# Kernel tuning notes

Hardware: AMD Instinct MI355X
Metric: run time of the kernel (lower is better)

The kernel has to match this reference:

```python
import jax, jax.numpy as jnp
import numpy as np

KSIZE = 3
STRIDE = 1
PADDING = 1
DILATION = 1
C_IN = 16
C_OUT = 16


def setup_inputs() -> dict:
    key = jax.random.key(0)
    k1, k2, k3 = jax.random.split(key, 3)
    inputs = jax.random.normal(k1, (2, C_IN, 24, 24, 24, 24), dtype=jnp.float32)
    weight = jax.random.normal(k2, (C_OUT, C_IN * KSIZE ** 4), dtype=jnp.float32)
    bias = jax.random.normal(k3, (1, C_OUT, 1, 1, 1, 1), dtype=jnp.float32)
    return {"inputs": inputs, "weight": weight, "bias": bias}


def reference(inputs, weight, bias):
    # weight stored flattened: [C_out, C_in * k^4] -> [C_out, C_in, k, k, k, k]
    w = weight.reshape(C_OUT, C_IN, KSIZE, KSIZE, KSIZE, KSIZE)
    # General 4-spatial-dim convolution via XLA's ND conv.
    dn = jax.lax.ConvDimensionNumbers(
        lhs_spec=(0, 1, 2, 3, 4, 5),   # N, C, U, V, H, W
        rhs_spec=(0, 1, 2, 3, 4, 5),   # O, I, kU, kV, kH, kW
        out_spec=(0, 1, 2, 3, 4, 5),
    )
    out = jax.lax.conv_general_dilated(
        inputs, w,
        window_strides=(STRIDE,) * 4,
        padding=((PADDING, PADDING),) * 4,
        rhs_dilation=(DILATION,) * 4,
        dimension_numbers=dn,
    )
    return out + bias
```

## Files before the change

kernel.cpp:

```cpp
#include <hip/hip_runtime.h>

#define S 24
#define PLANE 576
#define CISTRIDE 331776
#define SLAB_B 21632
#define HSLAB_B 11648
#define HOFF 9984
#define A_BYTES 46080
#define WS_SLABS A_BYTES

typedef __attribute__((ext_vector_type(8))) short bf16x8;
typedef __attribute__((ext_vector_type(4))) float f32x4;

__device__ __forceinline__ ushort f2bf(float f) {
    unsigned int u = __builtin_bit_cast(unsigned int, f);
    unsigned int r = u + 0x7fffu + ((u >> 16) & 1u);
    return (ushort)(r >> 16);
}

__device__ __forceinline__ int swz(int row, int col, int half) {
    return (((row * 26 + col) * 32) + half * 16) ^ ((row & 3) << 4);
}

__global__ void __launch_bounds__(256)
pack_in(const float* __restrict__ in, const float* __restrict__ wgt, char* __restrict__ ws) {
    __shared__ unsigned lds_t[16][288];

    const int b = blockIdx.x;
    const int nb = b / PLANE, uv = b % PLANE;
    const float* src = in + (size_t)nb * 16 * CISTRIDE + (size_t)uv * PLANE;
    char* dst = ws + WS_SLABS + (size_t)b * SLAB_B;
    const int t = threadIdx.x;

    #pragma unroll
    for (int i = 0; i < 9; ++i) {
        int flat = i * 256 + t;
        int ci = flat / 144, q4 = flat % 144;
        float4 f = *(const float4*)(src + (size_t)ci * CISTRIDE + 4 * q4);
        uint2 pk;
        pk.x = (unsigned)f2bf(f.x) | ((unsigned)f2bf(f.y) << 16);
        pk.y = (unsigned)f2bf(f.z) | ((unsigned)f2bf(f.w) << 16);
        *(uint2*)&lds_t[ci][2 * q4] = pk;
    }
    __syncthreads();

    #pragma unroll
    for (int i = 0; i < 6; ++i) {
        int c = i * 256 + t;
        if (c < 1352) {
            int k = c >> 2;
            int row = k / 13;
            int pos2 = c ^ (row & 3);
            int pos = pos2 >> 1, h = pos2 & 1;
            int col = pos - row * 26;
            uint4 o = make_uint4(0, 0, 0, 0);
            if (row >= 1 && row <= 24 && col >= 1 && col <= 24) {
                int q = (row - 1) * 24 + (col - 1);
                int q2 = q >> 1, odd = q & 1;
                #pragma unroll
                for (int kk = 0; kk < 4; ++kk) {
                    unsigned a = lds_t[8 * h + 2 * kk][q2];
                    unsigned bb = lds_t[8 * h + 2 * kk + 1][q2];
                    unsigned val = odd ? ((a >> 16) | (bb & 0xffff0000u))
                                       : ((a & 0xffffu) | (bb << 16));
                    ((unsigned*)&o)[kk] = val;
                }
            }
            *(uint4*)(dst + (size_t)c * 16) = o;
        }
    }

    if (b == 0) {
        for (int i = t; i < 2880; i += 256) {
            int step = i >> 6;
            int tap = step / 5, s = step % 5;
            int lane = i & 63;
            int co = lane & 15, gA = lane >> 4;
            int o = 2 * s + (gA >> 1);
            int cib = (gA & 1) * 8;
            ushort vals[8];
            #pragma unroll
            for (int j = 0; j < 8; ++j)
                vals[j] = (o <= 8) ? f2bf(wgt[co * 1296 + (cib + j) * 81 + tap * 9 + o]) : (ushort)0;
            uint4 pk;
            pk.x = vals[0] | ((unsigned)vals[1] << 16);
            pk.y = vals[2] | ((unsigned)vals[3] << 16);
            pk.z = vals[4] | ((unsigned)vals[5] << 16);
            pk.w = vals[6] | ((unsigned)vals[7] << 16);
            *(uint4*)(ws + (size_t)i * 16) = pk;
        }
    }
}

__global__ void __launch_bounds__(192, 4)
conv4d_main(const char* __restrict__ ws, const float* __restrict__ bias,
            float* __restrict__ out) {
    __shared__ __align__(16) char lds[2 * HSLAB_B];

    const int t = threadIdx.x, lane = t & 63, wvid = t >> 6;
    const int braw = blockIdx.x;
    const int b = (braw & 7) * 144 + (braw >> 3);
    const int nb = b / 576, rem = b % 576;
    const int u = rem / 24, rem2 = rem % 24;
    const int v0 = (rem2 >> 1) * 2, hh = rem2 & 1;

    const int n16 = lane & 15, g = lane >> 4;
    const int dh = n16 >> 3, dw = n16 & 7;
    const int half = g & 1, osel = g >> 1;

    int laneoff[2][5];
    #pragma unroll
    for (int trp = 0; trp < 2; ++trp)
        #pragma unroll
        for (int s = 0; s < 5; ++s) {
            int o = 2 * s + osel; if (o > 8) o = 8;
            int kh = o / 3, kw = o % 3;
            int r_off = dh + kh, c_off = dw + kw;
            int lin = (r_off * 26 + c_off) * 32 + half * 16;
            laneoff[trp][s] = lin ^ ((((trp << 1) + r_off) & 3) << 4);
        }

    f32x4 acc0[6], acc1[6];
    #pragma unroll
    for (int i = 0; i < 6; ++i) { acc0[i] = (f32x4){0,0,0,0}; acc1[i] = (f32x4){0,0,0,0}; }

    unsigned mask = 0;
    #pragma unroll
    for (int i = 0; i < 12; ++i) {
        int uu = u + (i >> 2) - 1, vv = v0 + (i & 3) - 1;
        if (uu >= 0 && uu < S && vv >= 0 && vv < S) mask |= 1u << i;
    }

    const char* slabs = ws + WS_SLABS;
    const int srcoff = hh * HOFF;
    #define SLAB_PTR(i_) (slabs + ((size_t)nb * PLANE + (u + ((i_) >> 2) - 1) * S + (v0 + ((i_) & 3) - 1)) * SLAB_B + srcoff)

    #define STAGE(bufsel_, src_) do {                                              \
        const char* _s = (src_);                                                   \
        _Pragma("unroll")                                                          \
        for (int r2 = 0; r2 < 4; ++r2) {                                           \
            int chunk = r2 * 192 + t;                                              \
            if (r2 < 3 || t < 152)                                                 \
                __builtin_amdgcn_global_load_lds(                                  \
                    (const __attribute__((address_space(1))) unsigned int*)(_s + (size_t)chunk * 16), \
                    (__attribute__((address_space(3))) unsigned int*)(lds + (bufsel_) * HSLAB_B + chunk * 16), \
                    16, 0, 0);                                                     \
        }                                                                          \
    } while (0)

    const bf16x8 zfr = {0,0,0,0,0,0,0,0};

    int cur = __ffs(mask) - 1;
    int bufsel = 0;
    STAGE(0, SLAB_PTR(cur));
    __syncthreads();

    while (1) {
        unsigned remm = mask >> (cur + 1);
        int nxt = remm ? (cur + 1 + __ffs(remm) - 1) : -1;
        if (nxt >= 0) STAGE(bufsel ^ 1, SLAB_PTR(nxt));

        const int ku = cur >> 2, dv = (cur & 3) - 1;
        const bool v0ok = dv <= 1, v1ok = dv >= 0;
        const char* ap0 = ws + (size_t)(ku * 3 + dv + 1) * 5120 + (size_t)lane * 16;
        const char* ap1 = ws + (size_t)(ku * 3 + dv) * 5120 + (size_t)lane * 16;
        bf16x8 afr0[5], afr1[5];
        #pragma unroll
        for (int s = 0; s < 5; ++s) {
            afr0[s] = v0ok ? *(const bf16x8*)(ap0 + s * 1024) : zfr;
            afr1[s] = v1ok ? *(const bf16x8*)(ap1 + s * 1024) : zfr;
        }

        const char* bp = lds + bufsel * HSLAB_B + wvid * 3328;
        #pragma unroll
        for (int tr = 0; tr < 2; ++tr) {
            #pragma unroll
            for (int tc = 0; tc < 3; ++tc) {
                const int ti = tr * 3 + tc;
                const char* bpt = bp + tr * 1664 + tc * 256;
                #pragma unroll
                for (int s = 0; s < 5; ++s) {
                    bf16x8 bfr = *(const bf16x8*)(bpt + laneoff[tr][s]);
                    acc0[ti] = __builtin_amdgcn_mfma_f32_16x16x32_bf16(afr0[s], bfr, acc0[ti], 0, 0, 0);
                    acc1[ti] = __builtin_amdgcn_mfma_f32_16x16x32_bf16(afr1[s], bfr, acc1[ti], 0, 0, 0);
                }
            }
        }
        __syncthreads();
        if (nxt < 0) break;
        cur = nxt; bufsel ^= 1;
    }

    float bv[4];
    #pragma unroll
    for (int r = 0; r < 4; ++r) bv[r] = bias[g * 4 + r];
    float* outp0 = out + (size_t)nb * 16 * CISTRIDE + (size_t)(u * S + v0) * PLANE;
    float* outp1 = outp0 + PLANE;
    #pragma unroll
    for (int tr = 0; tr < 2; ++tr) {
        #pragma unroll
        for (int tc = 0; tc < 3; ++tc) {
            const int ti = tr * 3 + tc;
            int row = hh * 12 + wvid * 4 + tr * 2 + dh;
            int col = tc * 8 + dw;
            int pos = row * S + col;
            #pragma unroll
            for (int r = 0; r < 4; ++r) {
                outp0[(size_t)(g * 4 + r) * CISTRIDE + pos] = acc0[ti][r] + bv[r];
                outp1[(size_t)(g * 4 + r) * CISTRIDE + pos] = acc1[ti][r] + bv[r];
            }
        }
    }
}

extern "C" void kernel_launch(void* const* d_in, const int* in_sizes, int n_in,
                              void* d_out, int out_size, void* d_ws, size_t ws_size,
                              hipStream_t stream) {
    const float* in   = (const float*)d_in[0];
    const float* wgt  = (const float*)d_in[1];
    const float* bias = (const float*)d_in[2];
    float* out        = (float*)d_out;
    char* ws          = (char*)d_ws;

    pack_in<<<dim3(2 * PLANE), dim3(256), 0, stream>>>(in, wgt, ws);
    conv4d_main<<<dim3(1152), dim3(192), 0, stream>>>(ws, bias, out);
}
```

Measured before the change: 77.43 us.

## Split conv work into quarter-slab tiles and half-plane pack blocks for more blocks

The main conv kernel now gives each block a quarter of the HW plane (6 output rows) instead of a half, doubling the grid to 2304 blocks and halving the per-block LDS slab and accumulator count. Each wave covers one 8-column strip across 3 row pairs instead of 2 rows by 3 column tiles. The pack kernel is likewise split so each block handles half a plane, doubling its grid and halving its LDS. This aims for better occupancy and load balance across CUs, at the cost of more redundant halo loading (quarter slabs overlap by halo rows) and more weight-fragment reloads per output.

Measured after the change: 79.18 us. 1.02x slower.

```diff
diff --git a/kernel.cpp b/kernel.cpp
--- a/kernel.cpp
+++ b/kernel.cpp
@@ -4,8 +4,8 @@
 #define PLANE 576
 #define CISTRIDE 331776
 #define SLAB_B 21632
-#define HSLAB_B 11648
-#define HOFF 9984
+#define QSLAB_B 6656
+#define QOFF 4992
 #define A_BYTES 46080
 #define WS_SLABS A_BYTES
 
@@ -18,45 +18,45 @@
     return (ushort)(r >> 16);
 }
 
-__device__ __forceinline__ int swz(int row, int col, int half) {
-    return (((row * 26 + col) * 32) + half * 16) ^ ((row & 3) << 4);
-}
-
 __global__ void __launch_bounds__(256)
 pack_in(const float* __restrict__ in, const float* __restrict__ wgt, char* __restrict__ ws) {
-    __shared__ unsigned lds_t[16][288];
+    __shared__ unsigned lds_t[16][144];
 
     const int b = blockIdx.x;
-    const int nb = b / PLANE, uv = b % PLANE;
-    const float* src = in + (size_t)nb * 16 * CISTRIDE + (size_t)uv * PLANE;
-    char* dst = ws + WS_SLABS + (size_t)b * SLAB_B;
+    const int slab = b >> 1, hhp = b & 1;
+    const int nb = slab / PLANE, uv = slab % PLANE;
+    const float* src = in + (size_t)nb * 16 * CISTRIDE + (size_t)uv * PLANE + hhp * 288;
+    char* dst = ws + WS_SLABS + (size_t)slab * SLAB_B;
     const int t = threadIdx.x;
 
     #pragma unroll
-    for (int i = 0; i < 9; ++i) {
+    for (int i = 0; i < 5; ++i) {
         int flat = i * 256 + t;
-        int ci = flat / 144, q4 = flat % 144;
-        float4 f = *(const float4*)(src + (size_t)ci * CISTRIDE + 4 * q4);
-        uint2 pk;
-        pk.x = (unsigned)f2bf(f.x) | ((unsigned)f2bf(f.y) << 16);
-        pk.y = (unsigned)f2bf(f.z) | ((unsigned)f2bf(f.w) << 16);
-        *(uint2*)&lds_t[ci][2 * q4] = pk;
+        if (flat < 1152) {
+            int ci = flat / 72, q4 = flat % 72;
+            float4 f = *(const float4*)(src + (size_t)ci * CISTRIDE + 4 * q4);
+            uint2 pk;
+            pk.x = (unsigned)f2bf(f.x) | ((unsigned)f2bf(f.y) << 16);
+            pk.y = (unsigned)f2bf(f.z) | ((unsigned)f2bf(f.w) << 16);
+            *(uint2*)&lds_t[ci][2 * q4] = pk;
+        }
     }
     __syncthreads();
 
     #pragma unroll
-    for (int i = 0; i < 6; ++i) {
+    for (int i = 0; i < 3; ++i) {
         int c = i * 256 + t;
-        if (c < 1352) {
-            int k = c >> 2;
-            int row = k / 13;
-            int pos2 = c ^ (row & 3);
+        if (c < 676) {
+            int row_local = c / 52;
+            int row = 13 * hhp + row_local;
+            int cg = 676 * hhp + c;
+            int pos2 = cg ^ (row & 3);
             int pos = pos2 >> 1, h = pos2 & 1;
             int col = pos - row * 26;
             uint4 o = make_uint4(0, 0, 0, 0);
             if (row >= 1 && row <= 24 && col >= 1 && col <= 24) {
-                int q = (row - 1) * 24 + (col - 1);
-                int q2 = q >> 1, odd = q & 1;
+                int ql = (row - 1) * 24 + (col - 1) - hhp * 288;
+                int q2 = ql >> 1, odd = ql & 1;
                 #pragma unroll
                 for (int kk = 0; kk < 4; ++kk) {
                     unsigned a = lds_t[8 * h + 2 * kk][q2];
@@ -66,7 +66,7 @@
                     ((unsigned*)&o)[kk] = val;
                 }
             }
-            *(uint4*)(dst + (size_t)c * 16) = o;
+            *(uint4*)(dst + (size_t)cg * 16) = o;
         }
     }
 
@@ -95,14 +95,14 @@
 __global__ void __launch_bounds__(192, 4)
 conv4d_main(const char* __restrict__ ws, const float* __restrict__ bias,
             float* __restrict__ out) {
-    __shared__ __align__(16) char lds[2 * HSLAB_B];
+    __shared__ __align__(16) char lds[2 * QSLAB_B];
 
     const int t = threadIdx.x, lane = t & 63, wvid = t >> 6;
     const int braw = blockIdx.x;
-    const int b = (braw & 7) * 144 + (braw >> 3);
-    const int nb = b / 576, rem = b % 576;
-    const int u = rem / 24, rem2 = rem % 24;
-    const int v0 = (rem2 >> 1) * 2, hh = rem2 & 1;
+    const int b = (braw & 7) * 288 + (braw >> 3);
+    const int nb = b / 1152, rem = b % 1152;
+    const int u = rem / 48, rem2 = rem % 48;
+    const int v0 = (rem2 >> 2) * 2, qq = rem2 & 3;
 
     const int n16 = lane & 15, g = lane >> 4;
     const int dh = n16 >> 3, dw = n16 & 7;
@@ -120,9 +120,9 @@
             laneoff[trp][s] = lin ^ ((((trp << 1) + r_off) & 3) << 4);
         }
 
-    f32x4 acc0[6], acc1[6];
-    #pragma unroll
-    for (int i = 0; i < 6; ++i) { acc0[i] = (f32x4){0,0,0,0}; acc1[i] = (f32x4){0,0,0,0}; }
+    f32x4 acc0[3], acc1[3];
+    #pragma unroll
+    for (int i = 0; i < 3; ++i) { acc0[i] = (f32x4){0,0,0,0}; acc1[i] = (f32x4){0,0,0,0}; }
 
     unsigned mask = 0;
     #pragma unroll
@@ -132,18 +132,18 @@
     }
 
     const char* slabs = ws + WS_SLABS;
-    const int srcoff = hh * HOFF;
+    const int srcoff = qq * QOFF;
     #define SLAB_PTR(i_) (slabs + ((size_t)nb * PLANE + (u + ((i_) >> 2) - 1) * S + (v0 + ((i_) & 3) - 1)) * SLAB_B + srcoff)
 
     #define STAGE(bufsel_, src_) do {                                              \
         const char* _s = (src_);                                                   \
         _Pragma("unroll")                                                          \
-        for (int r2 = 0; r2 < 4; ++r2) {                                           \
+        for (int r2 = 0; r2 < 3; ++r2) {                                           \
             int chunk = r2 * 192 + t;                                              \
-            if (r2 < 3 || t < 152)                                                 \
+            if (r2 < 2 || t < 32)                                                  \
                 __builtin_amdgcn_global_load_lds(                                  \
                     (const __attribute__((address_space(1))) unsigned int*)(_s + (size_t)chunk * 16), \
-                    (__attribute__((address_space(3))) unsigned int*)(lds + (bufsel_) * HSLAB_B + chunk * 16), \
+                    (__attribute__((address_space(3))) unsigned int*)(lds + (bufsel_) * QSLAB_B + chunk * 16), \
                     16, 0, 0);                                                     \
         }                                                                          \
     } while (0)
@@ -171,19 +171,16 @@
             afr1[s] = v1ok ? *(const bf16x8*)(ap1 + s * 1024) : zfr;
         }
 
-        const char* bp = lds + bufsel * HSLAB_B + wvid * 3328;
-        #pragma unroll
-        for (int tr = 0; tr < 2; ++tr) {
+        const char* bp = lds + bufsel * QSLAB_B + wvid * 256;
+        #pragma unroll
+        for (int tr = 0; tr < 3; ++tr) {
+            const int trp = (tr + qq) & 1;
+            const char* bpt = bp + tr * 1664;
             #pragma unroll
-            for (int tc = 0; tc < 3; ++tc) {
-                const int ti = tr * 3 + tc;
-                const char* bpt = bp + tr * 1664 + tc * 256;
-                #pragma unroll
-                for (int s = 0; s < 5; ++s) {
-                    bf16x8 bfr = *(const bf16x8*)(bpt + laneoff[tr][s]);
-                    acc0[ti] = __builtin_amdgcn_mfma_f32_16x16x32_bf16(afr0[s], bfr, acc0[ti], 0, 0, 0);
-                    acc1[ti] = __builtin_amdgcn_mfma_f32_16x16x32_bf16(afr1[s], bfr, acc1[ti], 0, 0, 0);
-                }
+            for (int s = 0; s < 5; ++s) {
+                bf16x8 bfr = *(const bf16x8*)(bpt + laneoff[trp][s]);
+                acc0[tr] = __builtin_amdgcn_mfma_f32_16x16x32_bf16(afr0[s], bfr, acc0[tr], 0, 0, 0);
+                acc1[tr] = __builtin_amdgcn_mfma_f32_16x16x32_bf16(afr1[s], bfr, acc1[tr], 0, 0, 0);
             }
         }
         __syncthreads();
@@ -197,18 +194,14 @@
     float* outp0 = out + (size_t)nb * 16 * CISTRIDE + (size_t)(u * S + v0) * PLANE;
     float* outp1 = outp0 + PLANE;
     #pragma unroll
-    for (int tr = 0; tr < 2; ++tr) {
-        #pragma unroll
-        for (int tc = 0; tc < 3; ++tc) {
-            const int ti = tr * 3 + tc;
-            int row = hh * 12 + wvid * 4 + tr * 2 + dh;
-            int col = tc * 8 + dw;
-            int pos = row * S + col;
-            #pragma unroll
-            for (int r = 0; r < 4; ++r) {
-                outp0[(size_t)(g * 4 + r) * CISTRIDE + pos] = acc0[ti][r] + bv[r];
-                outp1[(size_t)(g * 4 + r) * CISTRIDE + pos] = acc1[ti][r] + bv[r];
-            }
+    for (int tr = 0; tr < 3; ++tr) {
+        int row = qq * 6 + tr * 2 + dh;
+        int col = wvid * 8 + dw;
+        int pos = row * S + col;
+        #pragma unroll
+        for (int r = 0; r < 4; ++r) {
+            outp0[(size_t)(g * 4 + r) * CISTRIDE + pos] = acc0[tr][r] + bv[r];
+            outp1[(size_t)(g * 4 + r) * CISTRIDE + pos] = acc1[tr][r] + bv[r];
         }
     }
 }
@@ -222,6 +215,6 @@
     float* out        = (float*)d_out;
     char* ws          = (char*)d_ws;
 
-    pack_in<<<dim3(2 * PLANE), dim3(256), 0, stream>>>(in, wgt, ws);
-    conv4d_main<<<dim3(1152), dim3(192), 0, stream>>>(ws, bias, out);
-}
+    pack_in<<<dim3(2304), dim3(256), 0, stream>>>(in, wgt, ws);
+    conv4d_main<<<dim3(2304), dim3(192), 0, stream>>>(ws, bias, out);
+}
```
